# Kernel optimization log

Hardware: AMD Instinct MI355X
Metric: run time of the kernel (lower is better)

The kernel has to match this reference:

```python
import jax, jax.numpy as jnp
import numpy as np

N = 100000
E = 3200000
IN_CH = 128


def gcn_conv(x, src, dst, W, b, n):
    # x' = D^{-1/2} (A + I) D^{-1/2} x W + b  (PyG GCNConv defaults)
    h = x @ W  # [N, out]
    ones = jnp.ones(src.shape[0], dtype=h.dtype)
    deg = jax.ops.segment_sum(ones, dst, num_segments=n)  # in-degree incl. self-loops
    dinv = jnp.where(deg > 0, jax.lax.rsqrt(deg), 0.0)
    norm = dinv[src] * dinv[dst]  # [E+N]
    msg = h[src] * norm[:, None]  # gather + scale
    out = jax.ops.segment_sum(msg, dst, num_segments=n)  # scatter-add
    return out + b


def setup_inputs() -> dict:
    key = jax.random.key(0)
    ks = jax.random.split(key, 16)
    x = jax.random.normal(ks[0], (N, IN_CH), dtype=jnp.float32)
    edge_index = jax.random.randint(ks[1], (2, E), 0, N, dtype=jnp.int64)

    def lin(kw, kb, fan_in, fan_out):
        bound = 1.0 / np.sqrt(fan_in)
        W = jax.random.uniform(kw, (fan_in, fan_out), jnp.float32, -bound, bound)
        b = jax.random.uniform(kb, (fan_out,), jnp.float32, -bound, bound)
        return W, b

    W1, b1 = lin(ks[2], ks[3], IN_CH, 64)
    W2, b2 = lin(ks[4], ks[5], 64, 64)
    lw1, lb1 = lin(ks[6], ks[7], 64, 64)
    lw2, lb2 = lin(ks[8], ks[9], 64, 32)
    lw3, lb3 = lin(ks[10], ks[11], 32, 1)
    return {"x": x, "edge_index": edge_index, "W1": W1, "b1": b1,
            "W2": W2, "b2": b2, "lw1": lw1, "lb1": lb1,
            "lw2": lw2, "lb2": lb2, "lw3": lw3, "lb3": lb3}


def reference(x, edge_index, W1, b1, W2, b2, lw1, lb1, lw2, lb2, lw3, lb3):
    n = x.shape[0]
    loop = jnp.arange(n, dtype=edge_index.dtype)
    src = jnp.concatenate([edge_index[0], loop])  # add self-loops
    dst = jnp.concatenate([edge_index[1], loop])
    h = gcn_conv(x, src, dst, W1, b1, n)
    h = gcn_conv(h, src, dst, W2, b2, n)
    h = jax.nn.relu(h @ lw1 + lb1)
    h = jax.nn.relu(h @ lw2 + lb2)
    return h @ lw3 + lb3
```

## Files before the change

kernel.cpp:

```cpp
#include <hip/hip_runtime.h>

#define IN_CH 128
#define HID 64
#define TILE 8192
#define B2SHIFT 10
#define B2NODES 1024

__global__ __launch_bounds__(256) void k_hist1(const int* __restrict__ dst,
                                               int* __restrict__ H, int E, int P) {
  __shared__ int cnt[1024];
  const int tid = threadIdx.x;
  for (int i = tid; i < P; i += 256) cnt[i] = 0;
  __syncthreads();
  const int base = blockIdx.x * TILE;
  const int end = min(base + TILE, E);
  for (int i = base + tid; i < end; i += 256)
    atomicAdd(&cnt[dst[i] >> B2SHIFT], 1);
  __syncthreads();
  for (int i = tid; i < P; i += 256) H[blockIdx.x * P + i] = cnt[i];
}

__global__ __launch_bounds__(256) void k_colscan(const int* __restrict__ H,
    int* __restrict__ Orel, int* __restrict__ colTot, int P, int NBLK) {
  __shared__ int s[512];
  const int b = blockIdx.x, tid = threadIdx.x;
  const int iA = tid, iB = tid + 256;
  int origA = (iA < NBLK) ? H[iA * P + b] : 0;
  int origB = (iB < NBLK) ? H[iB * P + b] : 0;
  s[iA] = origA; s[iB] = origB;
  __syncthreads();
  for (int off = 1; off < 512; off <<= 1) {
    int tA = (iA >= off) ? s[iA - off] : 0;
    int tB = (iB >= off) ? s[iB - off] : 0;
    __syncthreads();
    s[iA] += tA; s[iB] += tB;
    __syncthreads();
  }
  if (iA < NBLK) Orel[iA * P + b] = s[iA] - origA;
  if (iB < NBLK) Orel[iB * P + b] = s[iB] - origB;
  if (tid == 255) colTot[b] = s[511];
}

__global__ __launch_bounds__(128) void k_bbase(const int* __restrict__ colTot,
                                               int* __restrict__ bBase, int P) {
  __shared__ int s[128];
  const int tid = threadIdx.x;
  int v = (tid < P) ? colTot[tid] : 0;
  s[tid] = v;
  __syncthreads();
  for (int off = 1; off < 128; off <<= 1) {
    int t = (tid >= off) ? s[tid - off] : 0;
    __syncthreads();
    s[tid] += t;
    __syncthreads();
  }
  if (tid < P) bBase[tid] = s[tid] - v;
  if (tid == P - 1) bBase[P] = s[tid];
}

__global__ __launch_bounds__(256) void k_pass1b(const int* __restrict__ src,
    const int* __restrict__ dst, const int* __restrict__ Orel,
    const int* __restrict__ bBase, unsigned* __restrict__ pairBuf, int E, int P) {
  __shared__ int off[1024], cur[1024];
  const int tid = threadIdx.x;
  for (int i = tid; i < P; i += 256) {
    off[i] = bBase[i] + Orel[blockIdx.x * P + i];
    cur[i] = 0;
  }
  __syncthreads();
  const int base = blockIdx.x * TILE;
  const int end = min(base + TILE, E);
  for (int i = base + tid; i < end; i += 256) {
    int d = dst[i];
    int b = d >> B2SHIFT;
    int r = atomicAdd(&cur[b], 1);
    pairBuf[off[b] + r] = ((unsigned)(d & (B2NODES - 1)) << 17) | (unsigned)src[i];
  }
}

__global__ __launch_bounds__(256) void k_pass2(const unsigned* __restrict__ pairBuf,
    const int* __restrict__ bBase, int* __restrict__ csr, int* __restrict__ rowptr,
    int* __restrict__ degInt, float* __restrict__ dinv, int N) {
  __shared__ int cnt[B2NODES], pfx[B2NODES], cur[B2NODES];
  __shared__ int lsum[256];
  const int b = blockIdx.x, tid = threadIdx.x;
  const int e0 = bBase[b], e1 = bBase[b + 1];
  for (int i = tid; i < B2NODES; i += 256) { cnt[i] = 0; cur[i] = 0; }
  __syncthreads();
  for (int i = e0 + tid; i < e1; i += 256)
    atomicAdd(&cnt[pairBuf[i] >> 17], 1);
  __syncthreads();
  int v[4], tsum = 0;
  #pragma unroll
  for (int k = 0; k < 4; ++k) { v[k] = cnt[tid * 4 + k]; tsum += v[k]; }
  lsum[tid] = tsum;
  __syncthreads();
  for (int off = 1; off < 256; off <<= 1) {
    int t = (tid >= off) ? lsum[tid - off] : 0;
    __syncthreads();
    lsum[tid] += t;
    __syncthreads();
  }
  int run = lsum[tid] - tsum;
  #pragma unroll
  for (int k = 0; k < 4; ++k) { pfx[tid * 4 + k] = run; run += v[k]; }
  __syncthreads();
  #pragma unroll
  for (int k = 0; k < 4; ++k) {
    int l = tid * 4 + k;
    int node = (b << B2SHIFT) + l;
    if (node < N) {
      rowptr[node] = e0 + pfx[l];
      degInt[node] = cnt[l];
      dinv[node]   = 1.0f / sqrtf((float)cnt[l] + 1.0f);
    }
  }
  __syncthreads();
  for (int i = e0 + tid; i < e1; i += 256) {
    unsigned u = pairBuf[i];
    int dl = u >> 17;
    int r = atomicAdd(&cur[dl], 1);
    csr[e0 + pfx[dl] + r] = (int)(u & 0x1FFFFu);
  }
}

__global__ __launch_bounds__(256) void k_gemm1(const float* __restrict__ x,
    const float* __restrict__ W1, const float* __restrict__ dinv,
    float* __restrict__ g1, int N) {
  __shared__ __align__(16) float Ws[IN_CH * HID];
  __shared__ __align__(16) float xs[64 * IN_CH];
  const int tid = threadIdx.x;
  const int base = blockIdx.x * 64;
  for (int i = tid; i < IN_CH * HID; i += 256) Ws[i] = W1[i];
  for (int i = tid; i < 64 * IN_CH; i += 256) {
    int row = i >> 7, col = i & 127;
    int n = base + row; if (n > N - 1) n = N - 1;
    xs[(row << 7) + (col ^ (row & 3))] = x[(size_t)n * IN_CH + col];
  }
  __syncthreads();
  const int w = tid >> 6, lane = tid & 63;
  const int ng = lane >> 4, cg = lane & 15;
  float acc[4][4];
  #pragma unroll
  for (int j = 0; j < 4; ++j)
    #pragma unroll
    for (int c = 0; c < 4; ++c) acc[j][c] = 0.f;
  #pragma unroll 8
  for (int k = 0; k < IN_CH; ++k) {
    float4 wv = *(const float4*)&Ws[(k << 6) + (cg << 2)];
    #pragma unroll
    for (int j = 0; j < 4; ++j) {
      int row = w * 16 + j * 4 + ng;
      float xv = xs[(row << 7) + (k ^ ng)];
      acc[j][0] = fmaf(xv, wv.x, acc[j][0]);
      acc[j][1] = fmaf(xv, wv.y, acc[j][1]);
      acc[j][2] = fmaf(xv, wv.z, acc[j][2]);
      acc[j][3] = fmaf(xv, wv.w, acc[j][3]);
    }
  }
  #pragma unroll
  for (int j = 0; j < 4; ++j) {
    int node = base + w * 16 + j * 4 + ng;
    if (node < N) {
      float di = dinv[node];
      float4 gv;
      gv.x = acc[j][0] * di; gv.y = acc[j][1] * di;
      gv.z = acc[j][2] * di; gv.w = acc[j][3] * di;
      *(float4*)&g1[(size_t)node * HID + (cg << 2)] = gv;
    }
  }
}

__global__ __launch_bounds__(256) void k_gemm2(const float* __restrict__ accIn,
    const float* __restrict__ W2, const float* __restrict__ b1,
    const float* __restrict__ dinv,
    float* __restrict__ g2, int N) {
  __shared__ __align__(16) float Ws[HID * HID];
  __shared__ __align__(16) float vs[64 * HID];
  const int tid = threadIdx.x;
  const int base = blockIdx.x * 64;
  for (int i = tid; i < HID * HID; i += 256) Ws[i] = W2[i];
  for (int i = tid; i < 64 * HID; i += 256) {
    int row = i >> 6, col = i & 63;
    int n = base + row; if (n > N - 1) n = N - 1;
    float v = fmaf(accIn[(size_t)n * HID + col], dinv[n], b1[col]);
    vs[(row << 6) + (col ^ (row & 3))] = v;
  }
  __syncthreads();
  const int w = tid >> 6, lane = tid & 63;
  const int ng = lane >> 4, cg = lane & 15;
  float acc[4][4];
  #pragma unroll
  for (int j = 0; j < 4; ++j)
    #pragma unroll
    for (int c = 0; c < 4; ++c) acc[j][c] = 0.f;
  #pragma unroll 8
  for (int k = 0; k < HID; ++k) {
    float4 wv = *(const float4*)&Ws[(k << 6) + (cg << 2)];
    #pragma unroll
    for (int j = 0; j < 4; ++j) {
      int row = w * 16 + j * 4 + ng;
      float xv = vs[(row << 6) + (k ^ ng)];
      acc[j][0] = fmaf(xv, wv.x, acc[j][0]);
      acc[j][1] = fmaf(xv, wv.y, acc[j][1]);
      acc[j][2] = fmaf(xv, wv.z, acc[j][2]);
      acc[j][3] = fmaf(xv, wv.w, acc[j][3]);
    }
  }
  #pragma unroll
  for (int j = 0; j < 4; ++j) {
    int node = base + w * 16 + j * 4 + ng;
    if (node < N) {
      float di = dinv[node];
      float4 gv;
      gv.x = acc[j][0] * di; gv.y = acc[j][1] * di;
      gv.z = acc[j][2] * di; gv.w = acc[j][3] * di;
      *(float4*)&g2[(size_t)node * HID + (cg << 2)] = gv;
    }
  }
}

__global__ __launch_bounds__(256) void k_gather(const int* __restrict__ rowptr,
    const int* __restrict__ degInt, const int* __restrict__ csr,
    const float* __restrict__ g, float* __restrict__ out, int N) {
  const int lane = threadIdx.x & 63;
  const int wid = (blockIdx.x * 256 + threadIdx.x) >> 6;
  if (wid >= N) return;
  const int start = rowptr[wid];
  const int deg = degInt[wid];
  float sum = g[(size_t)wid * HID + lane];
  for (int c = 0; c < deg; c += 64) {
    int rem = deg - c;
    int cnt = rem < 64 ? rem : 64;
    int idx = 0;
    if (lane < cnt) idx = csr[start + c + lane];
    int j = 0;
    for (; j + 8 <= cnt; j += 8) {
      int s0 = __shfl(idx, j, 64);
      int s1 = __shfl(idx, j + 1, 64);
      int s2 = __shfl(idx, j + 2, 64);
      int s3 = __shfl(idx, j + 3, 64);
      int s4 = __shfl(idx, j + 4, 64);
      int s5 = __shfl(idx, j + 5, 64);
      int s6 = __shfl(idx, j + 6, 64);
      int s7 = __shfl(idx, j + 7, 64);
      float a0 = g[(size_t)s0 * HID + lane];
      float a1 = g[(size_t)s1 * HID + lane];
      float a2 = g[(size_t)s2 * HID + lane];
      float a3 = g[(size_t)s3 * HID + lane];
      float a4 = g[(size_t)s4 * HID + lane];
      float a5 = g[(size_t)s5 * HID + lane];
      float a6 = g[(size_t)s6 * HID + lane];
      float a7 = g[(size_t)s7 * HID + lane];
      sum += a0; sum += a1; sum += a2; sum += a3;
      sum += a4; sum += a5; sum += a6; sum += a7;
    }
    for (; j + 4 <= cnt; j += 4) {
      int s0 = __shfl(idx, j, 64);
      int s1 = __shfl(idx, j + 1, 64);
      int s2 = __shfl(idx, j + 2, 64);
      int s3 = __shfl(idx, j + 3, 64);
      float a0 = g[(size_t)s0 * HID + lane];
      float a1 = g[(size_t)s1 * HID + lane];
      float a2 = g[(size_t)s2 * HID + lane];
      float a3 = g[(size_t)s3 * HID + lane];
      sum += a0; sum += a1; sum += a2; sum += a3;
    }
    for (; j < cnt; ++j)
      sum += g[(size_t)__shfl(idx, j, 64) * HID + lane];
  }
  out[(size_t)wid * HID + lane] = sum;
}

__global__ __launch_bounds__(256) void k_mlp(const float* __restrict__ accIn,
    const float* __restrict__ dinv, const float* __restrict__ b2,
    const float* __restrict__ lw1, const float* __restrict__ lb1,
    const float* __restrict__ lw2, const float* __restrict__ lb2,
    const float* __restrict__ lw3, const float* __restrict__ lb3,
    float* __restrict__ out, int N) {
  __shared__ __align__(16) float w1s[64 * 64];
  __shared__ __align__(16) float w2s[64 * 32];
  __shared__ float w3s[32], lb1s[64], lb2s[32];
  __shared__ __align__(16) float vs[64 * 64];
  __shared__ __align__(16) float t1s[64 * 64];
  const int tid = threadIdx.x;
  const int base = blockIdx.x * 64;
  for (int i = tid; i < 4096; i += 256) w1s[i] = lw1[i];
  for (int i = tid; i < 2048; i += 256) w2s[i] = lw2[i];
  if (tid < 64) lb1s[tid] = lb1[tid];
  if (tid < 32) { w3s[tid] = lw3[tid]; lb2s[tid] = lb2[tid]; }
  const float lb3v = lb3[0];
  for (int i = tid; i < 64 * 64; i += 256) {
    int row = i >> 6, col = i & 63;
    int n = base + row; if (n > N - 1) n = N - 1;
    vs[(row << 6) + (col ^ (row & 3))] = fmaf(accIn[(size_t)n * HID + col], dinv[n], b2[col]);
  }
  __syncthreads();
  const int w = tid >> 6, lane = tid & 63;
  const int ng = lane >> 4, cg = lane & 15;
  float acc[4][4];
  #pragma unroll
  for (int j = 0; j < 4; ++j)
    #pragma unroll
    for (int c = 0; c < 4; ++c) acc[j][c] = lb1s[(cg << 2) + c];
  #pragma unroll 8
  for (int k = 0; k < 64; ++k) {
    float4 wv = *(const float4*)&w1s[(k << 6) + (cg << 2)];
    #pragma unroll
    for (int j = 0; j < 4; ++j) {
      int row = w * 16 + j * 4 + ng;
      float xv = vs[(row << 6) + (k ^ ng)];
      acc[j][0] = fmaf(xv, wv.x, acc[j][0]);
      acc[j][1] = fmaf(xv, wv.y, acc[j][1]);
      acc[j][2] = fmaf(xv, wv.z, acc[j][2]);
      acc[j][3] = fmaf(xv, wv.w, acc[j][3]);
    }
  }
  #pragma unroll
  for (int j = 0; j < 4; ++j) {
    int row = w * 16 + j * 4 + ng;
    #pragma unroll
    for (int c = 0; c < 4; ++c)
      t1s[(row << 6) + (((cg << 2) + c) ^ ng)] = fmaxf(acc[j][c], 0.f);
  }
  __syncthreads();
  float a2[4][2];
  #pragma unroll
  for (int j = 0; j < 4; ++j) {
    a2[j][0] = lb2s[(cg << 1)];
    a2[j][1] = lb2s[(cg << 1) + 1];
  }
  #pragma unroll 8
  for (int k = 0; k < 64; ++k) {
    float2 wv = *(const float2*)&w2s[(k << 5) + (cg << 1)];
    #pragma unroll
    for (int j = 0; j < 4; ++j) {
      int row = w * 16 + j * 4 + ng;
      float xv = t1s[(row << 6) + (k ^ ng)];
      a2[j][0] = fmaf(xv, wv.x, a2[j][0]);
      a2[j][1] = fmaf(xv, wv.y, a2[j][1]);
    }
  }
  const float w3a = w3s[(cg << 1)], w3b = w3s[(cg << 1) + 1];
  #pragma unroll
  for (int j = 0; j < 4; ++j) {
    float p = fmaxf(a2[j][0], 0.f) * w3a + fmaxf(a2[j][1], 0.f) * w3b;
    p += __shfl_xor(p, 1, 64);
    p += __shfl_xor(p, 2, 64);
    p += __shfl_xor(p, 4, 64);
    p += __shfl_xor(p, 8, 64);
    int node = base + w * 16 + j * 4 + ng;
    if (cg == 0 && node < N) out[node] = p + lb3v;
  }
}

extern "C" void kernel_launch(void* const* d_in, const int* in_sizes, int n_in,
                              void* d_out, int out_size, void* d_ws, size_t ws_size,
                              hipStream_t stream) {
  const float* x   = (const float*)d_in[0];
  const int*   ei  = (const int*)d_in[1];
  const float* W1  = (const float*)d_in[2];
  const float* b1  = (const float*)d_in[3];
  const float* W2  = (const float*)d_in[4];
  const float* b2  = (const float*)d_in[5];
  const float* lw1 = (const float*)d_in[6];
  const float* lb1 = (const float*)d_in[7];
  const float* lw2 = (const float*)d_in[8];
  const float* lb2 = (const float*)d_in[9];
  const float* lw3 = (const float*)d_in[10];
  const float* lb3 = (const float*)d_in[11];
  float* out = (float*)d_out;

  const int N = in_sizes[0] / IN_CH;
  const int E = in_sizes[1] / 2;
  const int* src = ei;
  const int* dst = ei + E;
  const int NBLK = (E + TILE - 1) / TILE;
  const int P = (N + B2NODES - 1) >> B2SHIFT;

  auto align256 = [](size_t v) { return (v + 255) & ~(size_t)255; };
  char* ws = (char*)d_ws;
  size_t nB = align256((size_t)N * 4);
  float* dinv   = (float*)ws;  ws += nB;
  int*   degInt = (int*)ws;    ws += nB;
  int*   rowptr = (int*)ws;    ws += nB;
  int*   H      = (int*)ws;    ws += align256((size_t)NBLK * P * 4);
  int*   Orel   = (int*)ws;    ws += align256((size_t)NBLK * P * 4);
  int*   colTot = (int*)ws;    ws += align256((size_t)P * 4);
  int*   bBase  = (int*)ws;    ws += align256((size_t)(P + 1) * 4);
  int*   csr    = (int*)ws;    ws += align256((size_t)E * 4);
  float* bufA   = (float*)ws;  ws += (size_t)N * HID * 4;
  float* bufB   = (float*)ws;
  unsigned* pairBuf = (unsigned*)bufB;

  const int gb  = (N + 63) / 64;
  const int gatherBlocks = (N * 64 + 255) / 256;

  hipLaunchKernelGGL(k_hist1,   dim3(NBLK), dim3(256), 0, stream, dst, H, E, P);
  hipLaunchKernelGGL(k_colscan, dim3(P), dim3(256), 0, stream, H, Orel, colTot, P, NBLK);
  hipLaunchKernelGGL(k_bbase,   dim3(1), dim3(128), 0, stream, colTot, bBase, P);
  hipLaunchKernelGGL(k_pass1b,  dim3(NBLK), dim3(256), 0, stream, src, dst, Orel, bBase, pairBuf, E, P);
  hipLaunchKernelGGL(k_pass2,   dim3(P), dim3(256), 0, stream, pairBuf, bBase,
                     csr, rowptr, degInt, dinv, N);

  hipLaunchKernelGGL(k_gemm1, dim3(gb), dim3(256), 0, stream, x, W1, dinv, bufA, N);
  hipLaunchKernelGGL(k_gather, dim3(gatherBlocks), dim3(256), 0, stream,
                     rowptr, degInt, csr, bufA, bufB, N);
  hipLaunchKernelGGL(k_gemm2, dim3(gb), dim3(256), 0, stream, bufB, W2, b1, dinv, bufA, N);
  hipLaunchKernelGGL(k_gather, dim3(gatherBlocks), dim3(256), 0, stream,
                     rowptr, degInt, csr, bufA, bufB, N);
  hipLaunchKernelGGL(k_mlp, dim3(gb), dim3(256), 0, stream,
                     bufB, dinv, b2, lw1, lb1, lw2, lb2, lw3, lb3, out, N);
}
```

Measured before the change: 538.4 us.

## Merge CSR build and first GEMM into one cooperative kernel, fuse gathers into GEMMs

Replaces the five CSR-construction launches plus the first GEMM with a single cooperative kernel of 256 blocks that uses grid-wide syncs between phases and grid-stride loops. It also fuses each neighbour gather into the following GEMM or MLP kernel, so the aggregated features stay in shared memory instead of being written to and re-read from global memory. The aim is to cut launch overhead and intermediate traffic. In exchange, the grid is capped at 256 blocks with a 64KB shared buffer, which limits occupancy for the histogram and GEMM phases, and per-node gathers inside GEMM blocks may balance load less evenly across waves.

After: 845.1 us. +57.0%, slower.

```diff
diff --git a/kernel.cpp b/kernel.cpp
--- a/kernel.cpp
+++ b/kernel.cpp
@@ -1,4 +1,6 @@
 #include <hip/hip_runtime.h>
+#include <hip/hip_cooperative_groups.h>
+namespace coop = cooperative_groups;
 
 #define IN_CH 128
 #define HID 64
@@ -6,229 +8,9 @@
 #define B2SHIFT 10
 #define B2NODES 1024
 
-__global__ __launch_bounds__(256) void k_hist1(const int* __restrict__ dst,
-                                               int* __restrict__ H, int E, int P) {
-  __shared__ int cnt[1024];
-  const int tid = threadIdx.x;
-  for (int i = tid; i < P; i += 256) cnt[i] = 0;
-  __syncthreads();
-  const int base = blockIdx.x * TILE;
-  const int end = min(base + TILE, E);
-  for (int i = base + tid; i < end; i += 256)
-    atomicAdd(&cnt[dst[i] >> B2SHIFT], 1);
-  __syncthreads();
-  for (int i = tid; i < P; i += 256) H[blockIdx.x * P + i] = cnt[i];
-}
-
-__global__ __launch_bounds__(256) void k_colscan(const int* __restrict__ H,
-    int* __restrict__ Orel, int* __restrict__ colTot, int P, int NBLK) {
-  __shared__ int s[512];
-  const int b = blockIdx.x, tid = threadIdx.x;
-  const int iA = tid, iB = tid + 256;
-  int origA = (iA < NBLK) ? H[iA * P + b] : 0;
-  int origB = (iB < NBLK) ? H[iB * P + b] : 0;
-  s[iA] = origA; s[iB] = origB;
-  __syncthreads();
-  for (int off = 1; off < 512; off <<= 1) {
-    int tA = (iA >= off) ? s[iA - off] : 0;
-    int tB = (iB >= off) ? s[iB - off] : 0;
-    __syncthreads();
-    s[iA] += tA; s[iB] += tB;
-    __syncthreads();
-  }
-  if (iA < NBLK) Orel[iA * P + b] = s[iA] - origA;
-  if (iB < NBLK) Orel[iB * P + b] = s[iB] - origB;
-  if (tid == 255) colTot[b] = s[511];
-}
-
-__global__ __launch_bounds__(128) void k_bbase(const int* __restrict__ colTot,
-                                               int* __restrict__ bBase, int P) {
-  __shared__ int s[128];
-  const int tid = threadIdx.x;
-  int v = (tid < P) ? colTot[tid] : 0;
-  s[tid] = v;
-  __syncthreads();
-  for (int off = 1; off < 128; off <<= 1) {
-    int t = (tid >= off) ? s[tid - off] : 0;
-    __syncthreads();
-    s[tid] += t;
-    __syncthreads();
-  }
-  if (tid < P) bBase[tid] = s[tid] - v;
-  if (tid == P - 1) bBase[P] = s[tid];
-}
-
-__global__ __launch_bounds__(256) void k_pass1b(const int* __restrict__ src,
-    const int* __restrict__ dst, const int* __restrict__ Orel,
-    const int* __restrict__ bBase, unsigned* __restrict__ pairBuf, int E, int P) {
-  __shared__ int off[1024], cur[1024];
-  const int tid = threadIdx.x;
-  for (int i = tid; i < P; i += 256) {
-    off[i] = bBase[i] + Orel[blockIdx.x * P + i];
-    cur[i] = 0;
-  }
-  __syncthreads();
-  const int base = blockIdx.x * TILE;
-  const int end = min(base + TILE, E);
-  for (int i = base + tid; i < end; i += 256) {
-    int d = dst[i];
-    int b = d >> B2SHIFT;
-    int r = atomicAdd(&cur[b], 1);
-    pairBuf[off[b] + r] = ((unsigned)(d & (B2NODES - 1)) << 17) | (unsigned)src[i];
-  }
-}
-
-__global__ __launch_bounds__(256) void k_pass2(const unsigned* __restrict__ pairBuf,
-    const int* __restrict__ bBase, int* __restrict__ csr, int* __restrict__ rowptr,
-    int* __restrict__ degInt, float* __restrict__ dinv, int N) {
-  __shared__ int cnt[B2NODES], pfx[B2NODES], cur[B2NODES];
-  __shared__ int lsum[256];
-  const int b = blockIdx.x, tid = threadIdx.x;
-  const int e0 = bBase[b], e1 = bBase[b + 1];
-  for (int i = tid; i < B2NODES; i += 256) { cnt[i] = 0; cur[i] = 0; }
-  __syncthreads();
-  for (int i = e0 + tid; i < e1; i += 256)
-    atomicAdd(&cnt[pairBuf[i] >> 17], 1);
-  __syncthreads();
-  int v[4], tsum = 0;
-  #pragma unroll
-  for (int k = 0; k < 4; ++k) { v[k] = cnt[tid * 4 + k]; tsum += v[k]; }
-  lsum[tid] = tsum;
-  __syncthreads();
-  for (int off = 1; off < 256; off <<= 1) {
-    int t = (tid >= off) ? lsum[tid - off] : 0;
-    __syncthreads();
-    lsum[tid] += t;
-    __syncthreads();
-  }
-  int run = lsum[tid] - tsum;
-  #pragma unroll
-  for (int k = 0; k < 4; ++k) { pfx[tid * 4 + k] = run; run += v[k]; }
-  __syncthreads();
-  #pragma unroll
-  for (int k = 0; k < 4; ++k) {
-    int l = tid * 4 + k;
-    int node = (b << B2SHIFT) + l;
-    if (node < N) {
-      rowptr[node] = e0 + pfx[l];
-      degInt[node] = cnt[l];
-      dinv[node]   = 1.0f / sqrtf((float)cnt[l] + 1.0f);
-    }
-  }
-  __syncthreads();
-  for (int i = e0 + tid; i < e1; i += 256) {
-    unsigned u = pairBuf[i];
-    int dl = u >> 17;
-    int r = atomicAdd(&cur[dl], 1);
-    csr[e0 + pfx[dl] + r] = (int)(u & 0x1FFFFu);
-  }
-}
-
-__global__ __launch_bounds__(256) void k_gemm1(const float* __restrict__ x,
-    const float* __restrict__ W1, const float* __restrict__ dinv,
-    float* __restrict__ g1, int N) {
-  __shared__ __align__(16) float Ws[IN_CH * HID];
-  __shared__ __align__(16) float xs[64 * IN_CH];
-  const int tid = threadIdx.x;
-  const int base = blockIdx.x * 64;
-  for (int i = tid; i < IN_CH * HID; i += 256) Ws[i] = W1[i];
-  for (int i = tid; i < 64 * IN_CH; i += 256) {
-    int row = i >> 7, col = i & 127;
-    int n = base + row; if (n > N - 1) n = N - 1;
-    xs[(row << 7) + (col ^ (row & 3))] = x[(size_t)n * IN_CH + col];
-  }
-  __syncthreads();
-  const int w = tid >> 6, lane = tid & 63;
-  const int ng = lane >> 4, cg = lane & 15;
-  float acc[4][4];
-  #pragma unroll
-  for (int j = 0; j < 4; ++j)
-    #pragma unroll
-    for (int c = 0; c < 4; ++c) acc[j][c] = 0.f;
-  #pragma unroll 8
-  for (int k = 0; k < IN_CH; ++k) {
-    float4 wv = *(const float4*)&Ws[(k << 6) + (cg << 2)];
-    #pragma unroll
-    for (int j = 0; j < 4; ++j) {
-      int row = w * 16 + j * 4 + ng;
-      float xv = xs[(row << 7) + (k ^ ng)];
-      acc[j][0] = fmaf(xv, wv.x, acc[j][0]);
-      acc[j][1] = fmaf(xv, wv.y, acc[j][1]);
-      acc[j][2] = fmaf(xv, wv.z, acc[j][2]);
-      acc[j][3] = fmaf(xv, wv.w, acc[j][3]);
-    }
-  }
-  #pragma unroll
-  for (int j = 0; j < 4; ++j) {
-    int node = base + w * 16 + j * 4 + ng;
-    if (node < N) {
-      float di = dinv[node];
-      float4 gv;
-      gv.x = acc[j][0] * di; gv.y = acc[j][1] * di;
-      gv.z = acc[j][2] * di; gv.w = acc[j][3] * di;
-      *(float4*)&g1[(size_t)node * HID + (cg << 2)] = gv;
-    }
-  }
-}
-
-__global__ __launch_bounds__(256) void k_gemm2(const float* __restrict__ accIn,
-    const float* __restrict__ W2, const float* __restrict__ b1,
-    const float* __restrict__ dinv,
-    float* __restrict__ g2, int N) {
-  __shared__ __align__(16) float Ws[HID * HID];
-  __shared__ __align__(16) float vs[64 * HID];
-  const int tid = threadIdx.x;
-  const int base = blockIdx.x * 64;
-  for (int i = tid; i < HID * HID; i += 256) Ws[i] = W2[i];
-  for (int i = tid; i < 64 * HID; i += 256) {
-    int row = i >> 6, col = i & 63;
-    int n = base + row; if (n > N - 1) n = N - 1;
-    float v = fmaf(accIn[(size_t)n * HID + col], dinv[n], b1[col]);
-    vs[(row << 6) + (col ^ (row & 3))] = v;
-  }
-  __syncthreads();
-  const int w = tid >> 6, lane = tid & 63;
-  const int ng = lane >> 4, cg = lane & 15;
-  float acc[4][4];
-  #pragma unroll
-  for (int j = 0; j < 4; ++j)
-    #pragma unroll
-    for (int c = 0; c < 4; ++c) acc[j][c] = 0.f;
-  #pragma unroll 8
-  for (int k = 0; k < HID; ++k) {
-    float4 wv = *(const float4*)&Ws[(k << 6) + (cg << 2)];
-    #pragma unroll
-    for (int j = 0; j < 4; ++j) {
-      int row = w * 16 + j * 4 + ng;
-      float xv = vs[(row << 6) + (k ^ ng)];
-      acc[j][0] = fmaf(xv, wv.x, acc[j][0]);
-      acc[j][1] = fmaf(xv, wv.y, acc[j][1]);
-      acc[j][2] = fmaf(xv, wv.z, acc[j][2]);
-      acc[j][3] = fmaf(xv, wv.w, acc[j][3]);
-    }
-  }
-  #pragma unroll
-  for (int j = 0; j < 4; ++j) {
-    int node = base + w * 16 + j * 4 + ng;
-    if (node < N) {
-      float di = dinv[node];
-      float4 gv;
-      gv.x = acc[j][0] * di; gv.y = acc[j][1] * di;
-      gv.z = acc[j][2] * di; gv.w = acc[j][3] * di;
-      *(float4*)&g2[(size_t)node * HID + (cg << 2)] = gv;
-    }
-  }
-}
-
-__global__ __launch_bounds__(256) void k_gather(const int* __restrict__ rowptr,
-    const int* __restrict__ degInt, const int* __restrict__ csr,
-    const float* __restrict__ g, float* __restrict__ out, int N) {
-  const int lane = threadIdx.x & 63;
-  const int wid = (blockIdx.x * 256 + threadIdx.x) >> 6;
-  if (wid >= N) return;
-  const int start = rowptr[wid];
-  const int deg = degInt[wid];
-  float sum = g[(size_t)wid * HID + lane];
+__device__ __forceinline__ float gather_row(const int* __restrict__ csr, int start, int deg,
+                                            const float* __restrict__ g, int lane) {
+  float sum = 0.f;
   for (int c = 0; c < deg; c += 64) {
     int rem = deg - c;
     int cnt = rem < 64 ? rem : 64;
@@ -269,11 +51,237 @@
     for (; j < cnt; ++j)
       sum += g[(size_t)__shfl(idx, j, 64) * HID + lane];
   }
-  out[(size_t)wid * HID + lane] = sum;
+  return sum;
 }
 
-__global__ __launch_bounds__(256) void k_mlp(const float* __restrict__ accIn,
-    const float* __restrict__ dinv, const float* __restrict__ b2,
+__global__ __launch_bounds__(256) void k_build(const int* __restrict__ src,
+    const int* __restrict__ dst, const float* __restrict__ x,
+    const float* __restrict__ W1, int* __restrict__ H, int* __restrict__ Orel,
+    int* __restrict__ colTot, unsigned* __restrict__ pairBuf,
+    int* __restrict__ csr, int* __restrict__ rowptr, int* __restrict__ degInt,
+    float* __restrict__ dinv, float* __restrict__ g1,
+    int N, int E, int nblk, int gb) {
+  coop::grid_group grid = coop::this_grid();
+  __shared__ __align__(16) float sh[16384];
+  const int tid = threadIdx.x;
+  const int P = (N + B2NODES - 1) >> B2SHIFT;
+
+  {
+    int* cnt = (int*)sh;
+    for (int t = blockIdx.x; t < nblk; t += gridDim.x) {
+      for (int i = tid; i < P; i += 256) cnt[i] = 0;
+      __syncthreads();
+      const int b0 = t * TILE;
+      const int b1e = min(b0 + TILE, E);
+      for (int i = b0 + tid; i < b1e; i += 256)
+        atomicAdd(&cnt[dst[i] >> B2SHIFT], 1);
+      __syncthreads();
+      for (int i = tid; i < P; i += 256) H[t * P + i] = cnt[i];
+      __syncthreads();
+    }
+  }
+  grid.sync();
+  if (blockIdx.x < P) {
+    int* s = (int*)sh;
+    const int b = blockIdx.x;
+    const int iA = tid, iB = tid + 256;
+    int origA = (iA < nblk) ? H[iA * P + b] : 0;
+    int origB = (iB < nblk) ? H[iB * P + b] : 0;
+    s[iA] = origA; s[iB] = origB;
+    __syncthreads();
+    for (int off = 1; off < 512; off <<= 1) {
+      int tA = (iA >= off) ? s[iA - off] : 0;
+      int tB = (iB >= off) ? s[iB - off] : 0;
+      __syncthreads();
+      s[iA] += tA; s[iB] += tB;
+      __syncthreads();
+    }
+    if (iA < nblk) Orel[iA * P + b] = s[iA] - origA;
+    if (iB < nblk) Orel[iB * P + b] = s[iB] - origB;
+    if (tid == 255) colTot[b] = s[511];
+  }
+  grid.sync();
+  {
+    int* bb  = (int*)sh;
+    int* off = (int*)sh + 128;
+    int* cur = (int*)sh + 1152;
+    int myv = 0;
+    if (tid < 128) { myv = (tid < P) ? colTot[tid] : 0; bb[tid] = myv; }
+    __syncthreads();
+    for (int o = 1; o < 128; o <<= 1) {
+      int t2 = (tid < 128 && tid >= o) ? bb[tid - o] : 0;
+      __syncthreads();
+      if (tid < 128) bb[tid] += t2;
+      __syncthreads();
+    }
+    if (tid < 128) bb[tid] -= myv;
+    __syncthreads();
+    for (int t = blockIdx.x; t < nblk; t += gridDim.x) {
+      for (int i = tid; i < P; i += 256) { off[i] = bb[i] + Orel[t * P + i]; cur[i] = 0; }
+      __syncthreads();
+      const int b0 = t * TILE;
+      const int b1e = min(b0 + TILE, E);
+      for (int i = b0 + tid; i < b1e; i += 256) {
+        int d = dst[i];
+        int b = d >> B2SHIFT;
+        int r = atomicAdd(&cur[b], 1);
+        pairBuf[off[b] + r] = ((unsigned)(d & (B2NODES - 1)) << 17) | (unsigned)src[i];
+      }
+      __syncthreads();
+    }
+  }
+  grid.sync();
+  if (blockIdx.x < P) {
+    int* bb   = (int*)sh;
+    int* cnt  = (int*)sh + 128;
+    int* pfx  = (int*)sh + 1152;
+    int* cur  = (int*)sh + 2176;
+    int* lsum = (int*)sh + 3200;
+    const int b = blockIdx.x;
+    const int e0 = bb[b], e1 = bb[b + 1];
+    for (int i = tid; i < B2NODES; i += 256) { cnt[i] = 0; cur[i] = 0; }
+    __syncthreads();
+    for (int i = e0 + tid; i < e1; i += 256)
+      atomicAdd(&cnt[pairBuf[i] >> 17], 1);
+    __syncthreads();
+    int v[4], tsum = 0;
+    #pragma unroll
+    for (int k = 0; k < 4; ++k) { v[k] = cnt[tid * 4 + k]; tsum += v[k]; }
+    lsum[tid] = tsum;
+    __syncthreads();
+    for (int off = 1; off < 256; off <<= 1) {
+      int t = (tid >= off) ? lsum[tid - off] : 0;
+      __syncthreads();
+      lsum[tid] += t;
+      __syncthreads();
+    }
+    int run = lsum[tid] - tsum;
+    #pragma unroll
+    for (int k = 0; k < 4; ++k) { pfx[tid * 4 + k] = run; run += v[k]; }
+    __syncthreads();
+    #pragma unroll
+    for (int k = 0; k < 4; ++k) {
+      int l = tid * 4 + k;
+      int node = (b << B2SHIFT) + l;
+      if (node < N) {
+        rowptr[node] = e0 + pfx[l];
+        degInt[node] = cnt[l];
+        dinv[node]   = 1.0f / sqrtf((float)cnt[l] + 1.0f);
+      }
+    }
+    __syncthreads();
+    for (int i = e0 + tid; i < e1; i += 256) {
+      unsigned u = pairBuf[i];
+      int dl = u >> 17;
+      int r = atomicAdd(&cur[dl], 1);
+      csr[e0 + pfx[dl] + r] = (int)(u & 0x1FFFFu);
+    }
+  }
+  grid.sync();
+  {
+    float* Ws = sh;
+    float* xs = sh + 8192;
+    for (int i = tid; i < IN_CH * HID; i += 256) Ws[i] = W1[i];
+    const int w = tid >> 6, lane = tid & 63;
+    const int ng = lane >> 4, cg_ = lane & 15;
+    for (int t = blockIdx.x; t < gb; t += gridDim.x) {
+      __syncthreads();
+      const int base = t * 64;
+      for (int i = tid; i < 64 * IN_CH; i += 256) {
+        int row = i >> 7, col = i & 127;
+        int n = base + row; if (n > N - 1) n = N - 1;
+        xs[(row << 7) + (col ^ (row & 3))] = x[(size_t)n * IN_CH + col];
+      }
+      __syncthreads();
+      float acc[4][4];
+      #pragma unroll
+      for (int j = 0; j < 4; ++j)
+        #pragma unroll
+        for (int c = 0; c < 4; ++c) acc[j][c] = 0.f;
+      #pragma unroll 8
+      for (int k = 0; k < IN_CH; ++k) {
+        float4 wv = *(const float4*)&Ws[(k << 6) + (cg_ << 2)];
+        #pragma unroll
+        for (int j = 0; j < 4; ++j) {
+          int row = w * 16 + j * 4 + ng;
+          float xv = xs[(row << 7) + (k ^ ng)];
+          acc[j][0] = fmaf(xv, wv.x, acc[j][0]);
+          acc[j][1] = fmaf(xv, wv.y, acc[j][1]);
+          acc[j][2] = fmaf(xv, wv.z, acc[j][2]);
+          acc[j][3] = fmaf(xv, wv.w, acc[j][3]);
+        }
+      }
+      #pragma unroll
+      for (int j = 0; j < 4; ++j) {
+        int node = base + w * 16 + j * 4 + ng;
+        if (node < N) {
+          float di = dinv[node];
+          float4 gv;
+          gv.x = acc[j][0] * di; gv.y = acc[j][1] * di;
+          gv.z = acc[j][2] * di; gv.w = acc[j][3] * di;
+          *(float4*)&g1[(size_t)node * HID + (cg_ << 2)] = gv;
+        }
+      }
+    }
+  }
+}
+
+__global__ __launch_bounds__(256) void k_gg2(const int* __restrict__ rowptr,
+    const int* __restrict__ degInt, const int* __restrict__ csr,
+    const float* __restrict__ g1, const float* __restrict__ dinv,
+    const float* __restrict__ b1, const float* __restrict__ W2,
+    float* __restrict__ g2, int N) {
+  __shared__ __align__(16) float Ws[HID * HID];
+  __shared__ __align__(16) float vs[64 * HID];
+  const int tid = threadIdx.x;
+  const int base = blockIdx.x * 64;
+  for (int i = tid; i < HID * HID; i += 256) Ws[i] = W2[i];
+  const int w = tid >> 6, lane = tid & 63;
+  const float b1v = b1[lane];
+  for (int j = 0; j < 16; ++j) {
+    int row = (w << 4) + j;
+    int n = base + row; if (n > N - 1) n = N - 1;
+    float sum = g1[(size_t)n * HID + lane]
+              + gather_row(csr, rowptr[n], degInt[n], g1, lane);
+    vs[(row << 6) + (lane ^ (row & 3))] = fmaf(sum, dinv[n], b1v);
+  }
+  __syncthreads();
+  const int ng = lane >> 4, cg_ = lane & 15;
+  float acc[4][4];
+  #pragma unroll
+  for (int j = 0; j < 4; ++j)
+    #pragma unroll
+    for (int c = 0; c < 4; ++c) acc[j][c] = 0.f;
+  #pragma unroll 8
+  for (int k = 0; k < HID; ++k) {
+    float4 wv = *(const float4*)&Ws[(k << 6) + (cg_ << 2)];
+    #pragma unroll
+    for (int j = 0; j < 4; ++j) {
+      int row = w * 16 + j * 4 + ng;
+      float xv = vs[(row << 6) + (k ^ ng)];
+      acc[j][0] = fmaf(xv, wv.x, acc[j][0]);
+      acc[j][1] = fmaf(xv, wv.y, acc[j][1]);
+      acc[j][2] = fmaf(xv, wv.z, acc[j][2]);
+      acc[j][3] = fmaf(xv, wv.w, acc[j][3]);
+    }
+  }
+  #pragma unroll
+  for (int j = 0; j < 4; ++j) {
+    int node = base + w * 16 + j * 4 + ng;
+    if (node < N) {
+      float di = dinv[node];
+      float4 gv;
+      gv.x = acc[j][0] * di; gv.y = acc[j][1] * di;
+      gv.z = acc[j][2] * di; gv.w = acc[j][3] * di;
+      *(float4*)&g2[(size_t)node * HID + (cg_ << 2)] = gv;
+    }
+  }
+}
+
+__global__ __launch_bounds__(256) void k_gmlp(const int* __restrict__ rowptr,
+    const int* __restrict__ degInt, const int* __restrict__ csr,
+    const float* __restrict__ g2, const float* __restrict__ dinv,
+    const float* __restrict__ b2,
     const float* __restrict__ lw1, const float* __restrict__ lb1,
     const float* __restrict__ lw2, const float* __restrict__ lb2,
     const float* __restrict__ lw3, const float* __restrict__ lb3,
@@ -290,22 +298,25 @@
   if (tid < 64) lb1s[tid] = lb1[tid];
   if (tid < 32) { w3s[tid] = lw3[tid]; lb2s[tid] = lb2[tid]; }
   const float lb3v = lb3[0];
-  for (int i = tid; i < 64 * 64; i += 256) {
-    int row = i >> 6, col = i & 63;
+  const int w = tid >> 6, lane = tid & 63;
+  const float b2v = b2[lane];
+  for (int j = 0; j < 16; ++j) {
+    int row = (w << 4) + j;
     int n = base + row; if (n > N - 1) n = N - 1;
-    vs[(row << 6) + (col ^ (row & 3))] = fmaf(accIn[(size_t)n * HID + col], dinv[n], b2[col]);
+    float sum = g2[(size_t)n * HID + lane]
+              + gather_row(csr, rowptr[n], degInt[n], g2, lane);
+    vs[(row << 6) + (lane ^ (row & 3))] = fmaf(sum, dinv[n], b2v);
   }
   __syncthreads();
-  const int w = tid >> 6, lane = tid & 63;
-  const int ng = lane >> 4, cg = lane & 15;
+  const int ng = lane >> 4, cg_ = lane & 15;
   float acc[4][4];
   #pragma unroll
   for (int j = 0; j < 4; ++j)
     #pragma unroll
-    for (int c = 0; c < 4; ++c) acc[j][c] = lb1s[(cg << 2) + c];
+    for (int c = 0; c < 4; ++c) acc[j][c] = lb1s[(cg_ << 2) + c];
   #pragma unroll 8
   for (int k = 0; k < 64; ++k) {
-    float4 wv = *(const float4*)&w1s[(k << 6) + (cg << 2)];
+    float4 wv = *(const float4*)&w1s[(k << 6) + (cg_ << 2)];
     #pragma unroll
     for (int j = 0; j < 4; ++j) {
       int row = w * 16 + j * 4 + ng;
@@ -321,18 +332,18 @@
     int row = w * 16 + j * 4 + ng;
     #pragma unroll
     for (int c = 0; c < 4; ++c)
-      t1s[(row << 6) + (((cg << 2) + c) ^ ng)] = fmaxf(acc[j][c], 0.f);
+      t1s[(row << 6) + (((cg_ << 2) + c) ^ ng)] = fmaxf(acc[j][c], 0.f);
   }
   __syncthreads();
   float a2[4][2];
   #pragma unroll
   for (int j = 0; j < 4; ++j) {
-    a2[j][0] = lb2s[(cg << 1)];
-    a2[j][1] = lb2s[(cg << 1) + 1];
+    a2[j][0] = lb2s[(cg_ << 1)];
+    a2[j][1] = lb2s[(cg_ << 1) + 1];
   }
   #pragma unroll 8
   for (int k = 0; k < 64; ++k) {
-    float2 wv = *(const float2*)&w2s[(k << 5) + (cg << 1)];
+    float2 wv = *(const float2*)&w2s[(k << 5) + (cg_ << 1)];
     #pragma unroll
     for (int j = 0; j < 4; ++j) {
       int row = w * 16 + j * 4 + ng;
@@ -341,7 +352,7 @@
       a2[j][1] = fmaf(xv, wv.y, a2[j][1]);
     }
   }
-  const float w3a = w3s[(cg << 1)], w3b = w3s[(cg << 1) + 1];
+  const float w3a = w3s[(cg_ << 1)], w3b = w3s[(cg_ << 1) + 1];
   #pragma unroll
   for (int j = 0; j < 4; ++j) {
     float p = fmaxf(a2[j][0], 0.f) * w3a + fmaxf(a2[j][1], 0.f) * w3b;
@@ -350,7 +361,7 @@
     p += __shfl_xor(p, 4, 64);
     p += __shfl_xor(p, 8, 64);
     int node = base + w * 16 + j * 4 + ng;
-    if (cg == 0 && node < N) out[node] = p + lb3v;
+    if (cg_ == 0 && node < N) out[node] = p + lb3v;
   }
 }
 
@@ -371,12 +382,13 @@
   const float* lb3 = (const float*)d_in[11];
   float* out = (float*)d_out;
 
-  const int N = in_sizes[0] / IN_CH;
-  const int E = in_sizes[1] / 2;
+  int N = in_sizes[0] / IN_CH;
+  int E = in_sizes[1] / 2;
   const int* src = ei;
   const int* dst = ei + E;
-  const int NBLK = (E + TILE - 1) / TILE;
-  const int P = (N + B2NODES - 1) >> B2SHIFT;
+  int NBLKv = (E + TILE - 1) / TILE;
+  int Pv    = (N + B2NODES - 1) >> B2SHIFT;
+  int gb    = (N + 63) / 64;
 
   auto align256 = [](size_t v) { return (v + 255) & ~(size_t)255; };
   char* ws = (char*)d_ws;
@@ -384,31 +396,23 @@
   float* dinv   = (float*)ws;  ws += nB;
   int*   degInt = (int*)ws;    ws += nB;
   int*   rowptr = (int*)ws;    ws += nB;
-  int*   H      = (int*)ws;    ws += align256((size_t)NBLK * P * 4);
-  int*   Orel   = (int*)ws;    ws += align256((size_t)NBLK * P * 4);
-  int*   colTot = (int*)ws;    ws += align256((size_t)P * 4);
-  int*   bBase  = (int*)ws;    ws += align256((size_t)(P + 1) * 4);
+  int*   H      = (int*)ws;    ws += align256((size_t)NBLKv * Pv * 4);
+  int*   Orel   = (int*)ws;    ws += align256((size_t)NBLKv * Pv * 4);
+  int*   colTot = (int*)ws;    ws += align256((size_t)Pv * 4);
   int*   csr    = (int*)ws;    ws += align256((size_t)E * 4);
   float* bufA   = (float*)ws;  ws += (size_t)N * HID * 4;
   float* bufB   = (float*)ws;
   unsigned* pairBuf = (unsigned*)bufB;
 
-  const int gb  = (N + 63) / 64;
-  const int gatherBlocks = (N * 64 + 255) / 256;
-
-  hipLaunchKernelGGL(k_hist1,   dim3(NBLK), dim3(256), 0, stream, dst, H, E, P);
-  hipLaunchKernelGGL(k_colscan, dim3(P), dim3(256), 0, stream, H, Orel, colTot, P, NBLK);
-  hipLaunchKernelGGL(k_bbase,   dim3(1), dim3(128), 0, stream, colTot, bBase, P);
-  hipLaunchKernelGGL(k_pass1b,  dim3(NBLK), dim3(256), 0, stream, src, dst, Orel, bBase, pairBuf, E, P);
-  hipLaunchKernelGGL(k_pass2,   dim3(P), dim3(256), 0, stream, pairBuf, bBase,
-                     csr, rowptr, degInt, dinv, N);
-
-  hipLaunchKernelGGL(k_gemm1, dim3(gb), dim3(256), 0, stream, x, W1, dinv, bufA, N);
-  hipLaunchKernelGGL(k_gather, dim3(gatherBlocks), dim3(256), 0, stream,
-                     rowptr, degInt, csr, bufA, bufB, N);
-  hipLaunchKernelGGL(k_gemm2, dim3(gb), dim3(256), 0, stream, bufB, W2, b1, dinv, bufA, N);
-  hipLaunchKernelGGL(k_gather, dim3(gatherBlocks), dim3(256), 0, stream,
-                     rowptr, degInt, csr, bufA, bufB, N);
-  hipLaunchKernelGGL(k_mlp, dim3(gb), dim3(256), 0, stream,
-                     bufB, dinv, b2, lw1, lb1, lw2, lb2, lw3, lb3, out, N);
+  void* args[] = { (void*)&src, (void*)&dst, (void*)&x, (void*)&W1, (void*)&H,
+                   (void*)&Orel, (void*)&colTot, (void*)&pairBuf, (void*)&csr,
+                   (void*)&rowptr, (void*)&degInt, (void*)&dinv, (void*)&bufA,
+                   (void*)&N, (void*)&E, (void*)&NBLKv, (void*)&gb };
+  hipLaunchCooperativeKernel((void*)k_build, dim3(256), dim3(256), args, 0, stream);
+
+  hipLaunchKernelGGL(k_gg2, dim3(gb), dim3(256), 0, stream,
+                     rowptr, degInt, csr, bufA, dinv, b1, W2, bufB, N);
+  hipLaunchKernelGGL(k_gmlp, dim3(gb), dim3(256), 0, stream,
+                     rowptr, degInt, csr, bufB, dinv, b2,
+                     lw1, lb1, lw2, lb2, lw3, lb3, out, N);
 }
```
